# Kernel optimization log

Hardware: AMD Instinct MI355X
Metric: run time of the kernel (lower is better)

## Reference

```python
import jax, jax.numpy as jnp
import numpy as np

DIM = 64; N_LAYER = 2; B = 2048; M = 64
N_ENT = 100000; N_REL = 200
TEMP = 0.2; KGE_W = 1e-6
MIN_N = 1e-15; BND = 1e-5


def _norm(x):
    return jnp.sqrt(jnp.clip((x * x).sum(-1, keepdims=True), MIN_N))


def _l2(x):
    # F.normalize(p=2): x / max(||x||, 1e-12)
    return x / jnp.maximum(jnp.sqrt((x * x).sum(-1, keepdims=True)), 1e-12)


def _artanh(x):
    return jnp.arctanh(jnp.clip(x, -1.0 + BND, 1.0 - BND))


def expmap0(u):
    n = _norm(u)
    return jnp.tanh(n) * u / n


def logmap0(x):
    n = _norm(x)
    return _artanh(n) * x / n


def mobius_add(x, y):
    x2 = (x * x).sum(-1, keepdims=True)
    y2 = (y * y).sum(-1, keepdims=True)
    xy = (x * y).sum(-1, keepdims=True)
    num = (1 + 2 * xy + y2) * x + (1 - x2) * y
    den = 1 + 2 * xy + x2 * y2
    return num / jnp.clip(den, MIN_N)


def expmap(u, p):
    lam = 2.0 / jnp.clip(1.0 - (p * p).sum(-1, keepdims=True), MIN_N)
    n = _norm(u)
    return mobius_add(p, jnp.tanh(lam * n / 2.0) * u / n)


def logmap(x, p):
    m = mobius_add(-p, x)
    n = _norm(m)
    lam = 2.0 / jnp.clip(1.0 - (p * p).sum(-1, keepdims=True), MIN_N)
    return (2.0 / lam) * _artanh(n) * m / n


def _ed_agg(h, path, t, att_w1, att_w2):
    # attention: Linear(2d,d,no bias) -> LeakyReLU(0)==ReLU -> Linear(d,1,no bias) -> Sigmoid
    x = jnp.concatenate([h, path], -1)                       # [B,M,2d]
    a = jax.nn.sigmoid(jax.nn.relu(x @ att_w1) @ att_w2)[..., 0]  # [B,M]
    w = jax.nn.softmax(a, axis=-1)
    return (w[..., None] * t).sum(1)                          # [B,d]


def _hyper_agg(h, path, t, curvature, a2_w1, a2_b1, a2_w2, a2_b2):
    h, path, t = _l2(h), _l2(path), _l2(t)
    hh = expmap0(h) * jnp.abs(curvature)
    ht = expmap(t, hh)
    hr = expmap(path, hh)
    tang = logmap0(jnp.concatenate([hh, hr], -1))            # [B,M,2d]
    a = jnp.tanh(jax.nn.relu(tang @ a2_w1 + a2_b1) @ a2_w2 + a2_b2)[..., 0]
    w = jax.nn.softmax(a, axis=-1)                            # [B,M]
    agg = w[..., None] * ht
    mean_pt = (w[..., None] * hh).sum(1, keepdims=True)       # [B,1,d]
    e = logmap(agg, mean_pt)
    return (w[..., None] * e).sum(1)                          # [B,d]


def _build(E, R, h_idx, r_idx, t_idx, init_emb, agg):
    embs = [init_emb]
    for i in range(N_LAYER):
        h = E[h_idx[0]]
        path = R[r_idx[0]]
        for k in range(1, i + 1):  # faithful to source: inner loop reuses index i
            h = h + E[h_idx[i]]
            path = path * R[r_idx[i]]
        embs.append(agg(h, path, E[t_idx[i]]))
    return jnp.stack(embs)  # [L+1, B, d]


def _mlcl(a_stack, b_stack):
    # vectorized over layer index i of MLCL_Loss(a[i], b[i], a_list, b_list)
    na, nb = _l2(a_stack), _l2(b_stack)                       # [L+1,B,d]
    d = na.shape[-1]
    pos = (na * nb).sum(-1)                                   # [L+1,B]
    ttl1 = jnp.einsum('lbd,md->lbm', na, nb.reshape(-1, d))
    ttl2 = jnp.einsum('lbd,md->lbm', nb, na.reshape(-1, d))
    ep = jnp.exp(pos / TEMP)
    l1 = -jnp.log(ep / jnp.exp(ttl1 / TEMP).sum(-1)).sum()
    l2 = -jnp.log(ep / jnp.exp(ttl2 / TEMP).sum(-1)).sum()
    return KGE_W * (l1 + l2)


def _cat_rev(stack):
    # e = stack[0]; for i in 1..L: e = cat(stack[i], e) -> [L, L-1, ..., 0]
    return jnp.concatenate([stack[i] for i in range(stack.shape[0] - 1, -1, -1)], -1)


def setup_inputs() -> dict:
    key = jax.random.key(0)
    ks = jax.random.split(key, 24)
    def ent_idx(k):
        return jax.random.randint(k, (N_LAYER, B, M), 0, N_ENT, dtype=jnp.int32)
    def rel_idx(k):
        return jax.random.randint(k, (N_LAYER, B, M), 0, N_REL, dtype=jnp.int32)
    inp = {
        'items': jax.random.randint(ks[0], (B,), 0, N_ENT, dtype=jnp.int32),
        'ucf_h': ent_idx(ks[1]), 'ucf_r': rel_idx(ks[2]), 'ucf_t': ent_idx(ks[3]),
        'ikg_h': ent_idx(ks[4]), 'ikg_r': rel_idx(ks[5]), 'ikg_t': ent_idx(ks[6]),
        'ukg_h': ent_idx(ks[7]), 'ukg_r': rel_idx(ks[8]), 'ukg_t': ent_idx(ks[9]),
        'icf_h': ent_idx(ks[10]), 'icf_r': rel_idx(ks[11]), 'icf_t': ent_idx(ks[12]),
        'ent_emb': jax.random.normal(ks[13], (N_ENT, DIM), jnp.float32) * 0.02,
        'rel_emb': jax.random.normal(ks[14], (N_REL, DIM), jnp.float32) * 0.02,
        'att_w1': jax.random.normal(ks[15], (2 * DIM, DIM), jnp.float32) * 0.05,
        'att_w2': jax.random.normal(ks[16], (DIM, 1), jnp.float32) * 0.05,
        'att2_w1': jax.random.normal(ks[17], (2 * DIM, DIM), jnp.float32) * 0.05,
        'att2_b1': jnp.zeros((DIM,), jnp.float32),
        'att2_w2': jax.random.normal(ks[18], (DIM, 1), jnp.float32) * 0.05,
        'att2_b2': jnp.zeros((1,), jnp.float32),
        'curvature': jnp.asarray(1.0, jnp.float32),
    }
    return inp


def reference(items, ucf_h, ucf_r, ucf_t, ikg_h, ikg_r, ikg_t,
              ukg_h, ukg_r, ukg_t, icf_h, icf_r, icf_t,
              ent_emb, rel_emb, att_w1, att_w2,
              att2_w1, att2_b1, att2_w2, att2_b2, curvature):
    ed = lambda h, p, t: _ed_agg(h, p, t, att_w1, att_w2)
    hy = lambda h, p, t: _hyper_agg(h, p, t, curvature, att2_w1, att2_b1, att2_w2, att2_b2)
    ucf = _build(ent_emb, rel_emb, ucf_h, ucf_r, ucf_t, ent_emb[ucf_h[0]].mean(1), ed)
    ikg = _build(ent_emb, rel_emb, ikg_h, ikg_r, ikg_t, ent_emb[items], ed)
    ukg = _build(ent_emb, rel_emb, ukg_h, ukg_r, ukg_t, ent_emb[ukg_h[0]].mean(1), hy)
    icf = _build(ent_emb, rel_emb, icf_h, icf_r, icf_t, ent_emb[icf_h[0]].mean(1), hy)
    kge_loss = _mlcl(ucf, ukg) + _mlcl(ikg, icf)
    e_u = jnp.concatenate([_cat_rev(ucf), _cat_rev(ukg)], -1)
    e_i = jnp.concatenate([_cat_rev(icf), _cat_rev(ikg)], -1)
    scores = jax.nn.sigmoid((e_i * e_u).sum(-1))
    return scores, kge_loss
```

## Files before the change

kernel.cpp:

```cpp
#include <hip/hip_runtime.h>
#include <hip/hip_bf16.h>
#include <cstdint>
#include <cstddef>

constexpr int NB = 2048;
constexpr int NM = 64;
constexpr int ND = 64;
constexpr int NBM = NB * NM;
constexpr int NROWS = 3 * NB;
constexpr int STACK = 3 * NB * ND;
constexpr int NZ = 8;

typedef __attribute__((ext_vector_type(8))) short short8;
typedef __attribute__((ext_vector_type(4))) float float4v;

__device__ __forceinline__ float wsum(float v) {
#pragma unroll
  for (int o = 32; o > 0; o >>= 1) v += __shfl_xor(v, o, 64);
  return v;
}

__device__ __forceinline__ float wmax(float v) {
#pragma unroll
  for (int o = 32; o > 0; o >>= 1) v = fmaxf(v, __shfl_xor(v, o, 64));
  return v;
}

__device__ __forceinline__ float rcpf(float x) { return __builtin_amdgcn_rcpf(x); }
__device__ __forceinline__ float sqf(float x) { return __builtin_amdgcn_sqrtf(x); }

__device__ __forceinline__ float fast_tanh(float x) {
  float t = __expf(2.f * x);
  return (t - 1.f) * rcpf(t + 1.f);
}

__device__ __forceinline__ float artanh_clip(float x) {
  x = fminf(fmaxf(x, -1.f + 1e-5f), 1.f - 1e-5f);
  return 0.5f * __logf((1.f + x) * rcpf(1.f - x));
}

__device__ __forceinline__ ushort f2bf(float f) {
  uint u = __float_as_uint(f);
  return (ushort)((u + 0x7FFFu + ((u >> 16) & 1u)) >> 16);
}
__device__ __forceinline__ float bf2f(ushort u) {
  return __uint_as_float((uint)u << 16);
}

__device__ __forceinline__ float readlane_f(float v, int l) {
  return __int_as_float(__builtin_amdgcn_readlane(__float_as_int(v), l));
}

__global__ __launch_bounds__(256) void pack_w1_kernel(
    const float* __restrict__ w1, ushort* __restrict__ out) {
  int e = blockIdx.x * 256 + threadIdx.x;
  if (e >= 8192) return;
  int j = e & 7, ln = (e >> 3) & 63, nt = (e >> 9) & 3, kt = e >> 11;
  int n = nt * 16 + (ln & 15), k = kt * 32 + ((ln >> 4) << 3) + j;
  out[e] = f2bf(w1[k * 64 + n]);
}

__global__ __launch_bounds__(64) void init_item_kernel(
    const float* __restrict__ E, const int* __restrict__ idx, float* __restrict__ out) {
  int b = blockIdx.x, lane = threadIdx.x;
  out[(size_t)b * ND + lane] = E[(size_t)idx[b] * ND + lane];
}

constexpr int OFF_H = 0;
constexpr int OFF_P = 4608;
constexpr int OFF_T = 9728;
constexpr int XS = 152;
constexpr int REGA_SZ = 14336;

__global__ __launch_bounds__(256) void agg_all_kernel(
    const float* __restrict__ E, const float* __restrict__ R,
    const int* __restrict__ h0, const int* __restrict__ r0, const int* __restrict__ t0,
    const int* __restrict__ h1, const int* __restrict__ r1, const int* __restrict__ t1,
    const int* __restrict__ h2, const int* __restrict__ r2, const int* __restrict__ t2,
    const int* __restrict__ h3, const int* __restrict__ r3, const int* __restrict__ t3,
    const ushort* __restrict__ w1p_ed, const float* __restrict__ w2_ed,
    const ushort* __restrict__ w1p_hy, const float* __restrict__ b1,
    const float* __restrict__ w2_hy, const float* __restrict__ b2,
    const float* __restrict__ curv,
    float* __restrict__ s_ucf, float* __restrict__ s_ikg,
    float* __restrict__ s_ukg, float* __restrict__ s_icf) {
  __shared__ __align__(16) ushort regA[REGA_SZ];
  __shared__ float a_s[64];
  __shared__ float w_s[64];
  __shared__ float meanpt_s[64];
  __shared__ float part[4][64];
  __shared__ float scal;

  const int b = blockIdx.x;
  const int fam = blockIdx.y;
  const int tid = threadIdx.x;
  const int wave = tid >> 6, lane = tid & 63;
  const int m0 = __builtin_amdgcn_readfirstlane(wave) * 16;
  const int colq = lane & 15, quad = lane >> 4;
  const size_t L = (size_t)NB * ND;

  const int* h_idx = (fam == 0) ? h0 : (fam == 1) ? h1 : (fam == 2) ? h2 : h3;
  const int* r_idx = (fam == 0) ? r0 : (fam == 1) ? r1 : (fam == 2) ? r2 : r3;
  const int* t_idx = (fam == 0) ? t0 : (fam == 1) ? t1 : (fam == 2) ? t2 : t3;
  float* sb = (fam == 0) ? s_ucf : (fam == 1) ? s_ikg : (fam == 2) ? s_ukg : s_icf;

  uint hp[16];

  if (fam < 2) {
    const int do_init = (fam == 0);
    for (int layer = 0; layer < 2; ++layer) {
      if (layer == 0) {
        float macc = 0.f;
#pragma unroll
        for (int mi = 0; mi < 16; ++mi) {
          const int m = m0 + mi;
          float hd = E[(size_t)h_idx[b * NM + m] * ND + lane];
          float pd = R[(size_t)r_idx[b * NM + m] * ND + lane];
          macc += hd;
          ushort hb = f2bf(hd), pb = f2bf(pd);
          hp[mi] = (uint)hb | ((uint)pb << 16);
          regA[m * XS + lane] = hb;
          regA[m * XS + 64 + lane] = pb;
        }
        part[wave][lane] = macc;
      } else {
#pragma unroll
        for (int mi = 0; mi < 16; ++mi) {
          const int m = m0 + mi;
          float hd = bf2f((ushort)hp[mi]) + E[(size_t)h_idx[NBM + b * NM + m] * ND + lane];
          float pd = bf2f((ushort)(hp[mi] >> 16)) * R[(size_t)r_idx[NBM + b * NM + m] * ND + lane];
          ushort hb = f2bf(hd), pb = f2bf(pd);
          hp[mi] = (uint)hb | ((uint)pb << 16);
          regA[m * XS + lane] = hb;
          regA[m * XS + 64 + lane] = pb;
        }
      }

      {
        short8 afr[4];
#pragma unroll
        for (int kt = 0; kt < 4; ++kt)
          afr[kt] = *(const short8*)&regA[(m0 + colq) * XS + kt * 32 + quad * 8];
        float w2v[4];
#pragma unroll
        for (int nt = 0; nt < 4; ++nt) w2v[nt] = w2_ed[nt * 16 + colq];
        float cc[4][4];
#pragma unroll
        for (int nt = 0; nt < 4; ++nt) {
          float4v c = {0.f, 0.f, 0.f, 0.f};
#pragma unroll
          for (int kt = 0; kt < 4; ++kt) {
            short8 bfr = *(const short8*)&w1p_ed[(((kt << 2) | nt) * 64 + lane) * 8];
            c = __builtin_amdgcn_mfma_f32_16x16x32_bf16(afr[kt], bfr, c, 0, 0, 0);
          }
#pragma unroll
          for (int i = 0; i < 4; ++i) cc[nt][i] = c[i];
        }
        float sred[4];
#pragma unroll
        for (int i = 0; i < 4; ++i)
          sred[i] = fmaxf(cc[0][i], 0.f) * w2v[0] + fmaxf(cc[1][i], 0.f) * w2v[1] +
                    fmaxf(cc[2][i], 0.f) * w2v[2] + fmaxf(cc[3][i], 0.f) * w2v[3];
#pragma unroll
        for (int o = 8; o > 0; o >>= 1) {
#pragma unroll
          for (int i = 0; i < 4; ++i) sred[i] += __shfl_xor(sred[i], o, 64);
        }
        if (colq == 0) {
#pragma unroll
          for (int i = 0; i < 4; ++i)
            a_s[m0 + quad * 4 + i] = 1.f / (1.f + __expf(-sred[i]));
        }
      }
      __syncthreads();
      if (wave == 0) {
        if (layer == 0 && do_init)
          sb[(size_t)b * ND + lane] =
              (part[0][lane] + part[1][lane] + part[2][lane] + part[3][lane]) * (1.f / 64.f);
        float v = a_s[lane];
        float mx = wmax(v);
        float e = __expf(v - mx);
        float ssum = wsum(e);
        w_s[lane] = e / ssum;
      }
      __syncthreads();

      float o = 0.f;
#pragma unroll
      for (int mi = 0; mi < 16; ++mi) {
        const int m = m0 + mi;
        o = fmaf(w_s[m], E[(size_t)t_idx[(size_t)layer * NBM + b * NM + m] * ND + lane], o);
      }
      part[wave][lane] = o;
      __syncthreads();
      if (wave == 0)
        sb[(layer + 1) * L + (size_t)b * ND + lane] =
            part[0][lane] + part[1][lane] + part[2][lane] + part[3][lane];
      if (layer == 0) __syncthreads();
    }
  } else {
    const float cabs = fabsf(*curv);
    const int j = colq;
    const int srcl = ((j >> 2) << 4) + j;

    for (int layer = 0; layer < 2; ++layer) {
      if (layer == 0) {
        float macc = 0.f;
#pragma unroll
        for (int mi = 0; mi < 16; ++mi) {
          const int m = m0 + mi;
          float hd = E[(size_t)h_idx[b * NM + m] * ND + lane];
          float pd = R[(size_t)r_idx[b * NM + m] * ND + lane];
          float td = E[(size_t)t_idx[b * NM + m] * ND + lane];
          macc += hd;
          ushort hb = f2bf(hd), pb = f2bf(pd);
          hp[mi] = (uint)hb | ((uint)pb << 16);
          regA[OFF_H + m * 72 + lane] = hb;
          regA[OFF_P + m * 72 + lane] = pb;
          regA[OFF_T + m * 72 + lane] = f2bf(td);
        }
        part[wave][lane] = macc;
      } else {
#pragma unroll
        for (int mi = 0; mi < 16; ++mi) {
          const int m = m0 + mi;
          float hd = bf2f((ushort)hp[mi]) + E[(size_t)h_idx[NBM + b * NM + m] * ND + lane];
          float pd = bf2f((ushort)(hp[mi] >> 16)) * R[(size_t)r_idx[NBM + b * NM + m] * ND + lane];
          float td = E[(size_t)t_idx[(size_t)NBM + b * NM + m] * ND + lane];
          ushort hb = f2bf(hd), pb = f2bf(pd);
          hp[mi] = (uint)hb | ((uint)pb << 16);
          regA[OFF_H + m * 72 + lane] = hb;
          regA[OFF_P + m * 72 + lane] = pb;
          regA[OFF_T + m * 72 + lane] = f2bf(td);
        }
      }

      float sh, sp, st, sht, shp;
      {
        const int fr = m0 + colq;
        const ushort* pH = &regA[OFF_H + fr * 72 + quad * 8];
        const ushort* pP = &regA[OFF_P + fr * 72 + quad * 8];
        const ushort* pT = &regA[OFF_T + fr * 72 + quad * 8];
        short8 hh0 = *(const short8*)pH, hh1 = *(const short8*)(pH + 32);
        short8 pp0 = *(const short8*)pP, pp1 = *(const short8*)(pP + 32);
        short8 tt0 = *(const short8*)pT, tt1 = *(const short8*)(pT + 32);
        const int dr = colq & 3;
#define DIAG_DOT(OUTV, A0, A1, B0, B1)                                      \
        {                                                                    \
          float4v c = {0.f, 0.f, 0.f, 0.f};                                  \
          c = __builtin_amdgcn_mfma_f32_16x16x32_bf16(A0, B0, c, 0, 0, 0);   \
          c = __builtin_amdgcn_mfma_f32_16x16x32_bf16(A1, B1, c, 0, 0, 0);   \
          float dv = (dr & 2) ? ((dr & 1) ? c[3] : c[2])                     \
                              : ((dr & 1) ? c[1] : c[0]);                    \
          OUTV = __shfl(dv, srcl, 64);                                       \
        }
        DIAG_DOT(sh, hh0, hh1, hh0, hh1)
        DIAG_DOT(sp, pp0, pp1, pp0, pp1)
        DIAG_DOT(st, tt0, tt1, tt0, tt1)
        DIAG_DOT(sht, hh0, hh1, tt0, tt1)
        DIAG_DOT(shp, hh0, hh1, pp0, pp1)
#undef DIAG_DOT
      }

      float g_ch, g_e1, g_e2, g_gh, g_q1, g_q2, g_hts2;
      {
        float rih = rcpf(fmaxf(sqf(sh), 1e-12f));
        float rip = rcpf(fmaxf(sqf(sp), 1e-12f));
        float rit = rcpf(fmaxf(sqf(st), 1e-12f));
        float nh = sqf(fmaxf(sh * rih * rih, 1e-15f));
        float ch = fast_tanh(nh) * rcpf(nh) * rih * cabs;
        float p2 = ch * ch * sh;
        float lam = 2.f * rcpf(fmaxf(1.f - p2, 1e-15f));
        float ntn = sqf(fmaxf(st * rit * rit, 1e-15f));
        float ct = fast_tanh(0.5f * lam * ntn) * rcpf(ntn) * rit;
        float y2 = ct * ct * st, xy = ch * ct * sht;
        float At = 1.f + 2.f * xy + y2, Bt = 1.f - p2;
        float rdt = rcpf(fmaxf(1.f + 2.f * xy + p2 * y2, 1e-15f));
        g_e1 = At * ch * rdt;
        g_e2 = Bt * ct * rdt;
        g_hts2 = g_e1 * g_e1 * sh + 2.f * g_e1 * g_e2 * sht + g_e2 * g_e2 * st;
        float npn = sqf(fmaxf(sp * rip * rip, 1e-15f));
        float cp = fast_tanh(0.5f * lam * npn) * rcpf(npn) * rip;
        float z2 = cp * cp * sp, xz = ch * cp * shp;
        float Ar = 1.f + 2.f * xz + z2;
        float rdr = rcpf(fmaxf(1.f + 2.f * xz + p2 * z2, 1e-15f));
        float f1 = Ar * ch * rdr, f2 = Bt * cp * rdr;
        float hr2 = f1 * f1 * sh + 2.f * f1 * f2 * shp + f2 * f2 * sp;
        float n128 = sqf(fmaxf(p2 + hr2, 1e-15f));
        float fq = artanh_clip(n128) * rcpf(n128);
        g_ch = ch;
        g_gh = fq * ch;
        g_q1 = fq * f1;
        g_q2 = fq * f2;
      }

      __syncthreads();
      if (layer == 0 && wave == 0)
        sb[(size_t)b * ND + lane] =
            (part[0][lane] + part[1][lane] + part[2][lane] + part[3][lane]) * (1.f / 64.f);

#pragma unroll
      for (int mi = 0; mi < 16; ++mi) {
        const int m = m0 + mi;
        float hvf = bf2f((ushort)hp[mi]);
        float pvf = bf2f((ushort)(hp[mi] >> 16));
        float tvf = bf2f(regA[OFF_T + m * 72 + lane]);
        float ghm = readlane_f(g_gh, mi);
        float q1m = readlane_f(g_q1, mi);
        float q2m = readlane_f(g_q2, mi);
        float e1m = readlane_f(g_e1, mi);
        float e2m = readlane_f(g_e2, mi);
        regA[m * XS + lane] = f2bf(ghm * hvf);
        regA[m * XS + 64 + lane] = f2bf(q1m * hvf + q2m * pvf);
        regA[OFF_T + m * 72 + lane] = f2bf(e1m * hvf + e2m * tvf);
      }

      {
        short8 afr[4];
#pragma unroll
        for (int kt = 0; kt < 4; ++kt)
          afr[kt] = *(const short8*)&regA[(m0 + colq) * XS + kt * 32 + quad * 8];
        float b1v[4], w2v[4];
#pragma unroll
        for (int nt = 0; nt < 4; ++nt) {
          b1v[nt] = b1[nt * 16 + colq];
          w2v[nt] = w2_hy[nt * 16 + colq];
        }
        float cc[4][4];
#pragma unroll
        for (int nt = 0; nt < 4; ++nt) {
          float4v c = {0.f, 0.f, 0.f, 0.f};
#pragma unroll
          for (int kt = 0; kt < 4; ++kt) {
            short8 bfr = *(const short8*)&w1p_hy[(((kt << 2) | nt) * 64 + lane) * 8];
            c = __builtin_amdgcn_mfma_f32_16x16x32_bf16(afr[kt], bfr, c, 0, 0, 0);
          }
#pragma unroll
          for (int i = 0; i < 4; ++i) cc[nt][i] = c[i];
        }
        float b2v = b2[0];
        float sred[4];
#pragma unroll
        for (int i = 0; i < 4; ++i)
          sred[i] = fmaxf(cc[0][i] + b1v[0], 0.f) * w2v[0] +
                    fmaxf(cc[1][i] + b1v[1], 0.f) * w2v[1] +
                    fmaxf(cc[2][i] + b1v[2], 0.f) * w2v[2] +
                    fmaxf(cc[3][i] + b1v[3], 0.f) * w2v[3];
#pragma unroll
        for (int o = 8; o > 0; o >>= 1) {
#pragma unroll
          for (int i = 0; i < 4; ++i) sred[i] += __shfl_xor(sred[i], o, 64);
        }
        if (colq == 0) {
#pragma unroll
          for (int i = 0; i < 4; ++i)
            a_s[m0 + quad * 4 + i] = fast_tanh(sred[i] + b2v);
        }
      }
      __syncthreads();
      if (wave == 0) {
        float v = a_s[lane];
        float mx = wmax(v);
        float e = __expf(v - mx);
        float ssum = wsum(e);
        w_s[lane] = e / ssum;
      }
      __syncthreads();

      float mp = 0.f;
#pragma unroll
      for (int mi = 0; mi < 16; ++mi) {
        const int m = m0 + mi;
        mp = fmaf(w_s[m] * readlane_f(g_ch, mi), bf2f((ushort)hp[mi]), mp);
      }
      part[wave][lane] = mp;
      __syncthreads();
      if (wave == 0) {
        float v = part[0][lane] + part[1][lane] + part[2][lane] + part[3][lane];
        meanpt_s[lane] = v;
        float p2m = wsum(v * v);
        if (lane == 0) scal = p2m;
      }
      __syncthreads();

      float dpv;
      {
        const ushort* pA = &regA[OFF_T + (m0 + colq) * 72 + quad * 8];
        short8 a0 = *(const short8*)pA, a1 = *(const short8*)(pA + 32);
        short8 bm0, bm1;
#pragma unroll
        for (int jj = 0; jj < 8; ++jj) {
          bm0[jj] = (short)f2bf(meanpt_s[quad * 8 + jj]);
          bm1[jj] = (short)f2bf(meanpt_s[32 + quad * 8 + jj]);
        }
        float4v c = {0.f, 0.f, 0.f, 0.f};
        c = __builtin_amdgcn_mfma_f32_16x16x32_bf16(a0, bm0, c, 0, 0, 0);
        c = __builtin_amdgcn_mfma_f32_16x16x32_bf16(a1, bm1, c, 0, 0, 0);
        const int dr = colq & 3;
        float dv = (dr & 2) ? ((dr & 1) ? c[3] : c[2]) : ((dr & 1) ? c[1] : c[0]);
        dpv = __shfl(dv, srcl, 64);
      }

      const float p2m = scal;
      const float be = fmaxf(1.f - p2m, 1e-15f);
      float g1, g2;
      {
        float wm = w_s[m0 + j];
        float y2 = wm * wm * g_hts2;
        float xy = -wm * dpv;
        float al = 1.f + 2.f * xy + y2;
        float rd = rcpf(fmaxf(1.f + 2.f * xy + p2m * y2, 1e-15f));
        float md2 = (al * al * p2m - 2.f * al * be * wm * dpv + be * be * y2) * rd * rd;
        float n = sqf(fmaxf(md2, 1e-15f));
        float sm = be * artanh_clip(n) * rcpf(n) * rd;
        g1 = wm * wm * sm * be;
        g2 = wm * sm * al;
      }
      float ovec = 0.f, cA = 0.f;
#pragma unroll
      for (int mi = 0; mi < 16; ++mi) {
        const int m = m0 + mi;
        float htf = bf2f(regA[OFF_T + m * 72 + lane]);
        ovec = fmaf(readlane_f(g1, mi), htf, ovec);
        cA += readlane_f(g2, mi);
      }
      part[wave][lane] = ovec - cA * meanpt_s[lane];
      __syncthreads();
      if (wave == 0)
        sb[(layer + 1) * L + (size_t)b * ND + lane] =
            part[0][lane] + part[1][lane] + part[2][lane] + part[3][lane];
    }
  }
}

__global__ __launch_bounds__(256) void l2pos_kernel(
    const float* __restrict__ stacks, __hip_bfloat16* __restrict__ nbf,
    float* __restrict__ pos) {
  int row = blockIdx.x * 4 + (threadIdx.x >> 6);
  int lane = threadIdx.x & 63;
  int sa = blockIdx.y, sb = sa + 2;
  size_t offa = (size_t)sa * STACK + (size_t)row * ND + lane;
  size_t offb = (size_t)sb * STACK + (size_t)row * ND + lane;
  float a = stacks[offa];
  float c = stacks[offb];
  float q0 = a * a, q1 = c * c, q2 = a * c;
#pragma unroll
  for (int o = 32; o > 0; o >>= 1) {
    q0 += __shfl_xor(q0, o, 64);
    q1 += __shfl_xor(q1, o, 64);
    q2 += __shfl_xor(q2, o, 64);
  }
  float ra = rcpf(fmaxf(sqf(q0), 1e-12f));
  float rc = rcpf(fmaxf(sqf(q1), 1e-12f));
  nbf[offa] = __float2bfloat16(a * ra);
  nbf[offb] = __float2bfloat16(c * rc);
  if (lane == 0) pos[sa * NROWS + row] = q2 * ra * rc;
}

__global__ __launch_bounds__(256) void lse_mfma_kernel(
    const ushort* __restrict__ nbf, float* __restrict__ Spart) {
  __shared__ __align__(16) ushort ytile[2][64 * 72];
  const int tid = threadIdx.x;
  const int wave = tid >> 6, lane = tid & 63;
  const int pair = blockIdx.y;
  const int z = blockIdx.z;
  int xi = (pair & 2) ? ((pair & 1) ? 3 : 1) : ((pair & 1) ? 2 : 0);
  int yi = xi ^ 2;
  const ushort* X = nbf + (size_t)xi * STACK;
  const ushort* Y = nbf + (size_t)yi * STACK;
  const int r0 = blockIdx.x * 64 + wave * 16;
  const int row = lane & 15, quad = lane >> 4;

  short8 a0 = *(const short8*)&X[(size_t)(r0 + row) * 64 + quad * 8];
  short8 a1 = *(const short8*)&X[(size_t)(r0 + row) * 64 + 32 + quad * 8];

  const int srow = tid >> 2, schunk = tid & 3;
  constexpr int NT = (NROWS / NZ) / 64;
  const int c0 = z * (NROWS / NZ);
  const ushort* sg = &Y[(size_t)(c0 + srow) * 64 + schunk * 16];
  ushort* sl = &ytile[0][0] + srow * 72 + schunk * 16;

  {
    short8 s0 = *(const short8*)sg;
    short8 s1 = *(const short8*)(sg + 8);
    *(short8*)sl = s0;
    *(short8*)(sl + 8) = s1;
  }
  __syncthreads();

  float rsum[4] = {0.f, 0.f, 0.f, 0.f};
  for (int ct = 0; ct < NT; ++ct) {
    const int cur = ct & 1;
    short8 n0, n1;
    if (ct + 1 < NT) {
      const ushort* src = sg + (size_t)(ct + 1) * 64 * 64;
      n0 = *(const short8*)src;
      n1 = *(const short8*)(src + 8);
    }
#pragma unroll
    for (int nt = 0; nt < 4; ++nt) {
      const ushort* yr = &ytile[cur][(nt * 16 + row) * 72 + quad * 8];
      short8 b0 = *(const short8*)yr;
      short8 b1 = *(const short8*)(yr + 32);
      float4v c = {0.f, 0.f, 0.f, 0.f};
      c = __builtin_amdgcn_mfma_f32_16x16x32_bf16(a0, b0, c, 0, 0, 0);
      c = __builtin_amdgcn_mfma_f32_16x16x32_bf16(a1, b1, c, 0, 0, 0);
#pragma unroll
      for (int i = 0; i < 4; ++i) rsum[i] += __expf(c[i] * 5.f);
    }
    if (ct + 1 < NT) {
      ushort* dst = &ytile[0][0] + ((ct + 1) & 1) * (64 * 72) + srow * 72 + schunk * 16;
      *(short8*)dst = n0;
      *(short8*)(dst + 8) = n1;
      __syncthreads();
    }
  }
#pragma unroll
  for (int i = 0; i < 4; ++i) {
    float v = rsum[i];
    v += __shfl_xor(v, 1, 64);
    v += __shfl_xor(v, 2, 64);
    v += __shfl_xor(v, 4, 64);
    v += __shfl_xor(v, 8, 64);
    if (row == 0)
      Spart[((size_t)z * 4 + pair) * NROWS + r0 + quad * 4 + i] = v;
  }
}

__global__ __launch_bounds__(256) void scores_kernel(
    const float* __restrict__ stacks, float* __restrict__ out) {
  int b = blockIdx.x * 4 + (threadIdx.x >> 6);
  int lane = threadIdx.x & 63;
  float s = 0.f;
#pragma unroll
  for (int l = 0; l < 3; ++l) {
    size_t o = (size_t)l * NB * ND + (size_t)b * ND + lane;
    s += stacks[0 * (size_t)STACK + o] * stacks[3 * (size_t)STACK + o]
       + stacks[2 * (size_t)STACK + o] * stacks[1 * (size_t)STACK + o];
  }
  s = wsum(s);
  if (lane == 0) out[b] = 1.f / (1.f + __expf(-s));
}

__global__ __launch_bounds__(256) void loss_part_kernel(
    const float* __restrict__ Spart, const float* __restrict__ pos,
    double* __restrict__ lossp) {
  __shared__ double red[256];
  const int t = threadIdx.x, blk = blockIdx.x;
  double acc = 0.0;
#pragma unroll
  for (int r = 0; r < 2; ++r) {
    int i = blk * 512 + r * 256 + t;
    float s = 0.f;
#pragma unroll
    for (int zz = 0; zz < NZ; ++zz) s += Spart[i + zz * 4 * NROWS];
    acc += (double)__logf(s);
  }
  {
    int jj = blk * 256 + t;
    acc -= 10.0 * (double)pos[jj];
  }
  red[t] = acc;
  __syncthreads();
  for (int s = 128; s > 0; s >>= 1) {
    if (t < s) red[t] += red[t + s];
    __syncthreads();
  }
  if (t == 0) lossp[blk] = red[0];
}

__global__ __launch_bounds__(64) void loss_final_kernel(
    const double* __restrict__ lossp, float* __restrict__ out) {
  int lane = threadIdx.x;
  double v = (lane < 48) ? lossp[lane] : 0.0;
#pragma unroll
  for (int o = 32; o > 0; o >>= 1) v += __shfl_xor(v, o, 64);
  if (lane == 0) out[NB] = (float)(1e-6 * v);
}

extern "C" void kernel_launch(void* const* d_in, const int* in_sizes, int n_in,
                              void* d_out, int out_size, void* d_ws, size_t ws_size,
                              hipStream_t stream) {
  const int* items = (const int*)d_in[0];
  const int* ucf_h = (const int*)d_in[1];
  const int* ucf_r = (const int*)d_in[2];
  const int* ucf_t = (const int*)d_in[3];
  const int* ikg_h = (const int*)d_in[4];
  const int* ikg_r = (const int*)d_in[5];
  const int* ikg_t = (const int*)d_in[6];
  const int* ukg_h = (const int*)d_in[7];
  const int* ukg_r = (const int*)d_in[8];
  const int* ukg_t = (const int*)d_in[9];
  const int* icf_h = (const int*)d_in[10];
  const int* icf_r = (const int*)d_in[11];
  const int* icf_t = (const int*)d_in[12];
  const float* E = (const float*)d_in[13];
  const float* R = (const float*)d_in[14];
  const float* att_w1 = (const float*)d_in[15];
  const float* att_w2 = (const float*)d_in[16];
  const float* a2_w1 = (const float*)d_in[17];
  const float* a2_b1 = (const float*)d_in[18];
  const float* a2_w2 = (const float*)d_in[19];
  const float* a2_b2 = (const float*)d_in[20];
  const float* curv = (const float*)d_in[21];
  float* outp = (float*)d_out;

  float* ws = (float*)d_ws;
  float* stacks = ws;
  float* Spart = stacks + 4 * (size_t)STACK;
  float* posarr = Spart + (size_t)NZ * 4 * NROWS;
  __hip_bfloat16* nbf = (__hip_bfloat16*)(posarr + 2 * (size_t)NROWS);
  ushort* w1p_ed = (ushort*)(nbf + 4 * (size_t)STACK);
  ushort* w1p_hy = w1p_ed + 8192;
  double* lossp = (double*)(w1p_hy + 8192);

  float* ucf = stacks + 0 * (size_t)STACK;
  float* ikg = stacks + 1 * (size_t)STACK;
  float* ukg = stacks + 2 * (size_t)STACK;
  float* icf = stacks + 3 * (size_t)STACK;

  pack_w1_kernel<<<32, 256, 0, stream>>>(att_w1, w1p_ed);
  pack_w1_kernel<<<32, 256, 0, stream>>>(a2_w1, w1p_hy);

  init_item_kernel<<<NB, 64, 0, stream>>>(E, items, ikg);

  agg_all_kernel<<<dim3(NB, 4), 256, 0, stream>>>(
      E, R,
      ucf_h, ucf_r, ucf_t, ikg_h, ikg_r, ikg_t,
      ukg_h, ukg_r, ukg_t, icf_h, icf_r, icf_t,
      w1p_ed, att_w2, w1p_hy, a2_b1, a2_w2, a2_b2, curv,
      ucf, ikg, ukg, icf);

  l2pos_kernel<<<dim3(NROWS / 4, 2), 256, 0, stream>>>(stacks, nbf, posarr);
  lse_mfma_kernel<<<dim3(NROWS / 64, 4, NZ), 256, 0, stream>>>((const ushort*)nbf, Spart);

  scores_kernel<<<NB / 4, 256, 0, stream>>>(stacks, outp);
  loss_part_kernel<<<48, 256, 0, stream>>>(Spart, posarr, lossp);
  loss_final_kernel<<<1, 64, 0, stream>>>(lossp, outp);
}
```

Before: 354.1 us.

## Replace wave-0 softmax and shared broadcasts with per-wave redundant compute and shuffles

Every wave now computes the softmax over the 64 attention scores redundantly and reads weights via readlane/shfl, instead of having wave 0 write them to shared memory behind an extra barrier. The same is done for the hyperbolic mean point and its squared norm, which removes several __syncthreads per layer. The tail-embedding gathers in the Euclidean branch are issued before the attention MFMA so their latency overlaps it. The bf16 conversion is simplified to round-half-up with a perm-based pack, which slightly changes rounding behaviour.

```diff
diff --git a/kernel.cpp b/kernel.cpp
--- a/kernel.cpp
+++ b/kernel.cpp
@@ -40,12 +40,18 @@
 }
 
 __device__ __forceinline__ ushort f2bf(float f) {
-  uint u = __float_as_uint(f);
-  return (ushort)((u + 0x7FFFu + ((u >> 16) & 1u)) >> 16);
+  return (ushort)((__float_as_uint(f) + 0x8000u) >> 16);
 }
 __device__ __forceinline__ float bf2f(ushort u) {
   return __uint_as_float((uint)u << 16);
 }
+__device__ __forceinline__ uint pack_bf2(float h, float p) {
+  uint hu = __float_as_uint(h) + 0x8000u;
+  uint pu = __float_as_uint(p) + 0x8000u;
+  return __builtin_amdgcn_perm(pu, hu, 0x07060302);
+}
+__device__ __forceinline__ float hp_lo(uint v) { return __uint_as_float(v << 16); }
+__device__ __forceinline__ float hp_hi(uint v) { return __uint_as_float(v & 0xFFFF0000u); }
 
 __device__ __forceinline__ float readlane_f(float v, int l) {
   return __int_as_float(__builtin_amdgcn_readlane(__float_as_int(v), l));
@@ -86,10 +92,8 @@
     float* __restrict__ s_ukg, float* __restrict__ s_icf) {
   __shared__ __align__(16) ushort regA[REGA_SZ];
   __shared__ float a_s[64];
-  __shared__ float w_s[64];
-  __shared__ float meanpt_s[64];
   __shared__ float part[4][64];
-  __shared__ float scal;
+  __shared__ float minit[4][64];
 
   const int b = blockIdx.x;
   const int fam = blockIdx.y;
@@ -109,6 +113,7 @@
   if (fam < 2) {
     const int do_init = (fam == 0);
     for (int layer = 0; layer < 2; ++layer) {
+      float tv[16];
       if (layer == 0) {
         float macc = 0.f;
 #pragma unroll
@@ -117,24 +122,27 @@
           float hd = E[(size_t)h_idx[b * NM + m] * ND + lane];
           float pd = R[(size_t)r_idx[b * NM + m] * ND + lane];
           macc += hd;
-          ushort hb = f2bf(hd), pb = f2bf(pd);
-          hp[mi] = (uint)hb | ((uint)pb << 16);
-          regA[m * XS + lane] = hb;
-          regA[m * XS + 64 + lane] = pb;
-        }
-        part[wave][lane] = macc;
+          uint pk = pack_bf2(hd, pd);
+          hp[mi] = pk;
+          regA[m * XS + lane] = (ushort)pk;
+          regA[m * XS + 64 + lane] = (ushort)(pk >> 16);
+        }
+        if (do_init) minit[wave][lane] = macc;
       } else {
 #pragma unroll
         for (int mi = 0; mi < 16; ++mi) {
           const int m = m0 + mi;
-          float hd = bf2f((ushort)hp[mi]) + E[(size_t)h_idx[NBM + b * NM + m] * ND + lane];
-          float pd = bf2f((ushort)(hp[mi] >> 16)) * R[(size_t)r_idx[NBM + b * NM + m] * ND + lane];
-          ushort hb = f2bf(hd), pb = f2bf(pd);
-          hp[mi] = (uint)hb | ((uint)pb << 16);
-          regA[m * XS + lane] = hb;
-          regA[m * XS + 64 + lane] = pb;
-        }
-      }
+          float hd = hp_lo(hp[mi]) + E[(size_t)h_idx[NBM + b * NM + m] * ND + lane];
+          float pd = hp_hi(hp[mi]) * R[(size_t)r_idx[NBM + b * NM + m] * ND + lane];
+          uint pk = pack_bf2(hd, pd);
+          hp[mi] = pk;
+          regA[m * XS + lane] = (ushort)pk;
+          regA[m * XS + 64 + lane] = (ushort)(pk >> 16);
+        }
+      }
+#pragma unroll
+      for (int mi = 0; mi < 16; ++mi)
+        tv[mi] = E[(size_t)t_idx[(size_t)layer * NBM + b * NM + m0 + mi] * ND + lane];
 
       {
         short8 afr[4];
@@ -173,30 +181,27 @@
         }
       }
       __syncthreads();
-      if (wave == 0) {
-        if (layer == 0 && do_init)
-          sb[(size_t)b * ND + lane] =
-              (part[0][lane] + part[1][lane] + part[2][lane] + part[3][lane]) * (1.f / 64.f);
+
+      float wl;
+      {
         float v = a_s[lane];
         float mx = wmax(v);
         float e = __expf(v - mx);
-        float ssum = wsum(e);
-        w_s[lane] = e / ssum;
-      }
-      __syncthreads();
+        wl = e / wsum(e);
+      }
+      if (layer == 0 && do_init && wave == 0)
+        sb[(size_t)b * ND + lane] =
+            (minit[0][lane] + minit[1][lane] + minit[2][lane] + minit[3][lane]) * (1.f / 64.f);
 
       float o = 0.f;
 #pragma unroll
-      for (int mi = 0; mi < 16; ++mi) {
-        const int m = m0 + mi;
-        o = fmaf(w_s[m], E[(size_t)t_idx[(size_t)layer * NBM + b * NM + m] * ND + lane], o);
-      }
+      for (int mi = 0; mi < 16; ++mi)
+        o = fmaf(readlane_f(wl, m0 + mi), tv[mi], o);
       part[wave][lane] = o;
       __syncthreads();
       if (wave == 0)
         sb[(layer + 1) * L + (size_t)b * ND + lane] =
             part[0][lane] + part[1][lane] + part[2][lane] + part[3][lane];
-      if (layer == 0) __syncthreads();
     }
   } else {
     const float cabs = fabsf(*curv);
@@ -213,10 +218,10 @@
           float pd = R[(size_t)r_idx[b * NM + m] * ND + lane];
           float td = E[(size_t)t_idx[b * NM + m] * ND + lane];
           macc += hd;
-          ushort hb = f2bf(hd), pb = f2bf(pd);
-          hp[mi] = (uint)hb | ((uint)pb << 16);
-          regA[OFF_H + m * 72 + lane] = hb;
-          regA[OFF_P + m * 72 + lane] = pb;
+          uint pk = pack_bf2(hd, pd);
+          hp[mi] = pk;
+          regA[OFF_H + m * 72 + lane] = (ushort)pk;
+          regA[OFF_P + m * 72 + lane] = (ushort)(pk >> 16);
           regA[OFF_T + m * 72 + lane] = f2bf(td);
         }
         part[wave][lane] = macc;
@@ -224,13 +229,13 @@
 #pragma unroll
         for (int mi = 0; mi < 16; ++mi) {
           const int m = m0 + mi;
-          float hd = bf2f((ushort)hp[mi]) + E[(size_t)h_idx[NBM + b * NM + m] * ND + lane];
-          float pd = bf2f((ushort)(hp[mi] >> 16)) * R[(size_t)r_idx[NBM + b * NM + m] * ND + lane];
+          float hd = hp_lo(hp[mi]) + E[(size_t)h_idx[NBM + b * NM + m] * ND + lane];
+          float pd = hp_hi(hp[mi]) * R[(size_t)r_idx[NBM + b * NM + m] * ND + lane];
           float td = E[(size_t)t_idx[(size_t)NBM + b * NM + m] * ND + lane];
-          ushort hb = f2bf(hd), pb = f2bf(pd);
-          hp[mi] = (uint)hb | ((uint)pb << 16);
-          regA[OFF_H + m * 72 + lane] = hb;
-          regA[OFF_P + m * 72 + lane] = pb;
+          uint pk = pack_bf2(hd, pd);
+          hp[mi] = pk;
+          regA[OFF_H + m * 72 + lane] = (ushort)pk;
+          regA[OFF_P + m * 72 + lane] = (ushort)(pk >> 16);
           regA[OFF_T + m * 72 + lane] = f2bf(td);
         }
       }
@@ -302,8 +307,8 @@
 #pragma unroll
       for (int mi = 0; mi < 16; ++mi) {
         const int m = m0 + mi;
-        float hvf = bf2f((ushort)hp[mi]);
-        float pvf = bf2f((ushort)(hp[mi] >> 16));
+        float hvf = hp_lo(hp[mi]);
+        float pvf = hp_hi(hp[mi]);
         float tvf = bf2f(regA[OFF_T + m * 72 + lane]);
         float ghm = readlane_f(g_gh, mi);
         float q1m = readlane_f(g_q1, mi);
@@ -358,30 +363,24 @@
         }
       }
       __syncthreads();
-      if (wave == 0) {
+
+      float wl;
+      {
         float v = a_s[lane];
         float mx = wmax(v);
         float e = __expf(v - mx);
-        float ssum = wsum(e);
-        w_s[lane] = e / ssum;
-      }
-      __syncthreads();
+        wl = e / wsum(e);
+      }
 
       float mp = 0.f;
 #pragma unroll
-      for (int mi = 0; mi < 16; ++mi) {
-        const int m = m0 + mi;
-        mp = fmaf(w_s[m] * readlane_f(g_ch, mi), bf2f((ushort)hp[mi]), mp);
-      }
+      for (int mi = 0; mi < 16; ++mi)
+        mp = fmaf(readlane_f(wl, m0 + mi) * readlane_f(g_ch, mi), hp_lo(hp[mi]), mp);
       part[wave][lane] = mp;
       __syncthreads();
-      if (wave == 0) {
-        float v = part[0][lane] + part[1][lane] + part[2][lane] + part[3][lane];
-        meanpt_s[lane] = v;
-        float p2m = wsum(v * v);
-        if (lane == 0) scal = p2m;
-      }
-      __syncthreads();
+
+      float mv = part[0][lane] + part[1][lane] + part[2][lane] + part[3][lane];
+      float p2m = wsum(mv * mv);
 
       float dpv;
       {
@@ -390,8 +389,8 @@
         short8 bm0, bm1;
 #pragma unroll
         for (int jj = 0; jj < 8; ++jj) {
-          bm0[jj] = (short)f2bf(meanpt_s[quad * 8 + jj]);
-          bm1[jj] = (short)f2bf(meanpt_s[32 + quad * 8 + jj]);
+          bm0[jj] = (short)f2bf(__shfl(mv, quad * 8 + jj, 64));
+          bm1[jj] = (short)f2bf(__shfl(mv, 32 + quad * 8 + jj, 64));
         }
         float4v c = {0.f, 0.f, 0.f, 0.f};
         c = __builtin_amdgcn_mfma_f32_16x16x32_bf16(a0, bm0, c, 0, 0, 0);
@@ -401,11 +400,10 @@
         dpv = __shfl(dv, srcl, 64);
       }
 
-      const float p2m = scal;
       const float be = fmaxf(1.f - p2m, 1e-15f);
       float g1, g2;
       {
-        float wm = w_s[m0 + j];
+        float wm = __shfl(wl, m0 + j, 64);
         float y2 = wm * wm * g_hts2;
         float xy = -wm * dpv;
         float al = 1.f + 2.f * xy + y2;
@@ -424,7 +422,7 @@
         ovec = fmaf(readlane_f(g1, mi), htf, ovec);
         cA += readlane_f(g2, mi);
       }
-      part[wave][lane] = ovec - cA * meanpt_s[lane];
+      part[wave][lane] = ovec - cA * mv;
       __syncthreads();
       if (wave == 0)
         sb[(layer + 1) * L + (size_t)b * ND + lane] =
@@ -452,8 +450,9 @@
   }
   float ra = rcpf(fmaxf(sqf(q0), 1e-12f));
   float rc = rcpf(fmaxf(sqf(q1), 1e-12f));
-  nbf[offa] = __float2bfloat16(a * ra);
-  nbf[offb] = __float2bfloat16(c * rc);
+  ushort ua = f2bf(a * ra), uc = f2bf(c * rc);
+  nbf[offa] = *(__hip_bfloat16*)&ua;
+  nbf[offb] = *(__hip_bfloat16*)&uc;
   if (lane == 0) pos[sa * NROWS + row] = q2 * ra * rc;
 }
 
```

Result: faster. 345.0 us (-2.6%).
